# Performance work log

Hardware: AMD Instinct MI355X
Metric: run time of the kernel (lower is better)

## Reference

```python
import jax, jax.numpy as jnp
import numpy as np

FP8_MAX = 448.0  # max finite value of float8_e4m3fn
F8 = jnp.float8_e4m3fn


def setup_inputs() -> dict:
    key = jax.random.key(0)
    kx, kw, kb = jax.random.split(key, 3)
    B, S, K, N = 4, 2048, 4096, 16384
    x = jax.random.normal(kx, (B, S, K), dtype=jnp.float32)
    # Pre-quantized symmetric per-tensor FP8 weight: simulate quantization of a
    # realistically initialized fp32 weight with scale ws.
    ws = jnp.float32(0.01)
    w_fp32 = jax.random.normal(kw, (N, K), dtype=jnp.float32) * 0.02
    weight = jnp.clip(w_fp32 / ws, -FP8_MAX, FP8_MAX).astype(F8)  # [N, K] fp8
    weight_scale = jnp.full((1,), ws, dtype=jnp.float32)  # per-tensor strategy
    bias = jax.random.normal(kb, (N,), dtype=jnp.float32) * 0.01
    return {"x": x, "weight": weight, "weight_scale": weight_scale, "bias": bias}


def reference(x, weight, weight_scale, bias):
    # Dynamic per-tensor fp8 quantization of the activation (torchao
    # _input_activation_quant_func_fp8 with PerTensor granularity):
    # (input_scale * weight_scale), plus bias.
    amax = jnp.max(jnp.abs(x))
    x_scale = jnp.maximum(amax, jnp.float32(1e-12)) / FP8_MAX
    xq = jnp.clip(x / x_scale, -FP8_MAX, FP8_MAX).astype(F8).astype(jnp.float32)
    w = weight.astype(jnp.float32)  # [N, K]
    out = jnp.einsum("bsk,nk->bsn", xq, w)  # [B, S, N]
    out = out * (x_scale * weight_scale[0]) + bias
    return out
```

## Files before the change

kernel.cpp:

```cpp
#include <hip/hip_runtime.h>
#include <hip/hip_fp8.h>
#include <hip/hip_fp16.h>
#include <stdint.h>

#define FP8_MAX_V 448.0f

typedef float f32x16 __attribute__((ext_vector_type(16)));
typedef int i32x4 __attribute__((ext_vector_type(4)));
typedef int i32x8 __attribute__((ext_vector_type(8)));

__device__ __forceinline__ uint8_t cvt_fp8(float v) {
    return __hip_cvt_float_to_fp8(fminf(fmaxf(v, -FP8_MAX_V), FP8_MAX_V),
                                  __HIP_SATFINITE, __HIP_E4M3);
}

__global__ void fp8lin_init(unsigned* amax_bits) {
    *amax_bits = 0u;
}

__global__ void fp8lin_amax(const float4* __restrict__ x, unsigned* __restrict__ amax_bits, long n4) {
    float m = 0.f;
    long stride = (long)gridDim.x * blockDim.x;
    for (long i = blockIdx.x * (long)blockDim.x + threadIdx.x; i < n4; i += stride) {
        float4 v = x[i];
        m = fmaxf(m, fmaxf(fmaxf(fabsf(v.x), fabsf(v.y)), fmaxf(fabsf(v.z), fabsf(v.w))));
    }
#pragma unroll
    for (int o = 32; o; o >>= 1) m = fmaxf(m, __shfl_xor(m, o));
    if ((threadIdx.x & 63) == 0) atomicMax(amax_bits, __float_as_uint(m));
}

__global__ void fp8lin_scales(const unsigned* __restrict__ amax_bits,
                              const float* __restrict__ wscale,
                              float* __restrict__ scales) {
    float xs = fmaxf(__uint_as_float(*amax_bits), 1e-12f) / FP8_MAX_V;
    scales[0] = xs;
    scales[1] = xs * wscale[0];
}

__global__ void fp8lin_probe(const uint32_t* __restrict__ w, unsigned* __restrict__ flag) {
    __shared__ unsigned s32, s16, s4;
    if (threadIdx.x == 0) { s32 = 0u; s16 = 0u; s4 = 0u; }
    __syncthreads();
    unsigned o32 = 0u, o16 = 0u, o4 = 0u;
    for (int i = threadIdx.x; i < 4096; i += 256) {
        uint32_t v = w[i];
        o32 |= v & 0x000FFFFFu;
        uint32_t h0 = v & 0xFFFFu, h1 = v >> 16;
        o16 |= (h0 & 0x7Fu) | (h1 & 0x7Fu);
        o4  |= (h0 & 0x0Fu) | (h1 & 0x0Fu);
    }
    atomicOr(&s32, o32); atomicOr(&s16, o16); atomicOr(&s4, o4);
    __syncthreads();
    if (threadIdx.x == 0)
        *flag = (s32 == 0u) ? 0u : (s16 == 0u) ? 1u : (s4 == 0u) ? 2u : 3u;
}

__global__ void fp8lin_convw(const void* __restrict__ wsrc, const unsigned* __restrict__ flag,
                             uchar4* __restrict__ wq, long n4) {
    unsigned f = *flag;
    if (f == 3u) return;
    long stride = (long)gridDim.x * blockDim.x;
    if (f == 0u) {
        const float4* src = (const float4*)wsrc;
        for (long i = blockIdx.x * (long)blockDim.x + threadIdx.x; i < n4; i += stride) {
            float4 v = src[i];
            uchar4 o;
            o.x = cvt_fp8(v.x); o.y = cvt_fp8(v.y); o.z = cvt_fp8(v.z); o.w = cvt_fp8(v.w);
            wq[i] = o;
        }
    } else if (f == 1u) {
        const __half2* src = (const __half2*)wsrc;
        for (long i = blockIdx.x * (long)blockDim.x + threadIdx.x; i < n4; i += stride) {
            __half2 v0 = src[2 * i], v1 = src[2 * i + 1];
            uchar4 o;
            o.x = cvt_fp8(__half2float(v0.x)); o.y = cvt_fp8(__half2float(v0.y));
            o.z = cvt_fp8(__half2float(v1.x)); o.w = cvt_fp8(__half2float(v1.y));
            wq[i] = o;
        }
    } else {
        const ushort2* src = (const ushort2*)wsrc;
        for (long i = blockIdx.x * (long)blockDim.x + threadIdx.x; i < n4; i += stride) {
            ushort2 v0 = src[2 * i], v1 = src[2 * i + 1];
            uchar4 o;
            o.x = cvt_fp8(__uint_as_float((uint32_t)v0.x << 16));
            o.y = cvt_fp8(__uint_as_float((uint32_t)v0.y << 16));
            o.z = cvt_fp8(__uint_as_float((uint32_t)v1.x << 16));
            o.w = cvt_fp8(__uint_as_float((uint32_t)v1.y << 16));
            wq[i] = o;
        }
    }
}

__global__ void fp8lin_quant(const float4* __restrict__ x, const float* __restrict__ scales,
                             uchar4* __restrict__ xq, long n4) {
    float s = scales[0];
    long stride = (long)gridDim.x * blockDim.x;
    for (long i = blockIdx.x * (long)blockDim.x + threadIdx.x; i < n4; i += stride) {
        float4 v = x[i];
        uchar4 o;
        o.x = cvt_fp8(v.x / s); o.y = cvt_fp8(v.y / s);
        o.z = cvt_fp8(v.z / s); o.w = cvt_fp8(v.w / s);
        xq[i] = o;
    }
}

#define BM 256
#define BN 128
#define BK 64
#define A_BYTES 16384
#define B_BYTES 8192
#define BUF_BYTES (A_BYTES + B_BYTES)
#define SMEM_BYTES (2 * BUF_BYTES)

__device__ __forceinline__ void gload16(const uint8_t* src, uint8_t* ldst) {
    __builtin_amdgcn_global_load_lds(
        (const __attribute__((address_space(1))) uint32_t*)(uintptr_t)src,
        (__attribute__((address_space(3))) uint32_t*)(uintptr_t)ldst, 16, 0, 0);
}

#define WAITVM(N) asm volatile("s_waitcnt vmcnt(" #N ")" ::: "memory")
#define BARRIER() do { asm volatile("" ::: "memory"); __builtin_amdgcn_s_barrier(); \
                       asm volatile("" ::: "memory"); } while (0)

#define LDFRAG(dst, base, off) do {                                    \
    i32x4 _lo = *(const i32x4*)((base) + (off));                       \
    i32x4 _hi = *(const i32x4*)((base) + ((off) ^ 16));                \
    dst[0] = _lo[0]; dst[1] = _lo[1]; dst[2] = _lo[2]; dst[3] = _lo[3];\
    dst[4] = _hi[0]; dst[5] = _hi[1]; dst[6] = _hi[2]; dst[7] = _hi[3];\
} while (0)

#define MFMA_MX(A, B, C) __builtin_amdgcn_mfma_scale_f32_32x32x64_f8f6f4( \
    (A), (B), (C), 0, 0, 0, (int)0x7f7f7f7f, 0, (int)0x7f7f7f7f)

__global__ __launch_bounds__(256, 2) void fp8lin_gemm(
    const uint8_t* __restrict__ Aq,
    const uint8_t* __restrict__ Wraw,
    const uint8_t* __restrict__ Wconv,
    const unsigned* __restrict__ flag,
    const float* __restrict__ scales,
    const float* __restrict__ bias,
    float* __restrict__ out,
    int M, int N, int K) {
    extern __shared__ __align__(16) uint8_t smem[];

    const uint8_t* __restrict__ Wq = (*flag == 3u) ? Wraw : Wconv;

    const int tid = threadIdx.x;
    const int wid = tid >> 6;
    const int lane = tid & 63;
    const int wm = wid >> 1;
    const int wn = wid & 1;

    const int nbx = gridDim.x;
    const int orig = blockIdx.y * nbx + blockIdx.x;
    const int cpx = (gridDim.x * gridDim.y) >> 3;
    const int swzb = (orig & 7) * cpx + (orig >> 3);
    const int brow = (swzb / nbx) * BM;
    const int bcol = (swzb % nbx) * BN;

    const uint8_t* srcA[4];
    const uint8_t* srcB[2];
#pragma unroll
    for (int j = 0; j < 4; ++j) {
        int c = tid + 256 * j;
        int r = c >> 2;
        int sc = ((c & 3) ^ ((r >> 1) & 3)) * 16;
        srcA[j] = Aq + (size_t)(brow + r) * K + sc;
    }
#pragma unroll
    for (int j = 0; j < 2; ++j) {
        int c = tid + 256 * j;
        int r = c >> 2;
        int sc = ((c & 3) ^ ((r >> 1) & 3)) * 16;
        srcB[j] = Wq + (size_t)(bcol + r) * K + sc;
    }
    const int ldsW = wid * 1024;

    const int l31 = lane & 31;
    const int q = lane >> 5;
    const int swzr = (l31 >> 1) & 3;
    const int posl = (2 * q) ^ swzr;
    const int offA = (wm * 128 + l31) * 64 + posl * 16;
    const int offB = (wn * 64 + l31) * 64 + posl * 16;

    f32x16 acc[4][2];
#pragma unroll
    for (int mi = 0; mi < 4; ++mi)
#pragma unroll
        for (int ni = 0; ni < 2; ++ni)
#pragma unroll
            for (int r = 0; r < 16; ++r) acc[mi][ni][r] = 0.0f;

    auto STAGE = [&](int t, int ib) {
        size_t k0 = (size_t)t * BK;
        uint8_t* base = smem + ib * BUF_BYTES;
        gload16(srcA[0] + k0, base + ldsW);
        gload16(srcA[1] + k0, base + ldsW + 4096);
        gload16(srcA[2] + k0, base + ldsW + 8192);
        gload16(srcA[3] + k0, base + ldsW + 12288);
        gload16(srcB[0] + k0, base + A_BYTES + ldsW);
        gload16(srcB[1] + k0, base + A_BYTES + ldsW + 4096);
    };

    auto COMPUTE = [&](int ib) {
        const uint8_t* bA = smem + ib * BUF_BYTES;
        const uint8_t* bB = bA + A_BYTES;
        i32x8 a0, a1, a2, a3, b0, b1;
        LDFRAG(a0, bA, offA);
        LDFRAG(a1, bA, offA + 2048);
        LDFRAG(b0, bB, offB);
        LDFRAG(b1, bB, offB + 2048);
        __builtin_amdgcn_s_setprio(1);
        acc[0][0] = MFMA_MX(a0, b0, acc[0][0]);
        acc[1][0] = MFMA_MX(a1, b0, acc[1][0]);
        acc[0][1] = MFMA_MX(a0, b1, acc[0][1]);
        acc[1][1] = MFMA_MX(a1, b1, acc[1][1]);
        __builtin_amdgcn_s_setprio(0);
        LDFRAG(a2, bA, offA + 4096);
        LDFRAG(a3, bA, offA + 6144);
        __builtin_amdgcn_s_setprio(1);
        acc[2][0] = MFMA_MX(a2, b0, acc[2][0]);
        acc[3][0] = MFMA_MX(a3, b0, acc[3][0]);
        acc[2][1] = MFMA_MX(a2, b1, acc[2][1]);
        acc[3][1] = MFMA_MX(a3, b1, acc[3][1]);
        __builtin_amdgcn_s_setprio(0);
    };

    const int NT = K / BK;
    STAGE(0, 0);
    int cur = 0;
    for (int t = 0; t < NT - 1; ++t) {
        STAGE(t + 1, cur ^ 1);
        WAITVM(6);
        BARRIER();
        COMPUTE(cur);
        BARRIER();
        cur ^= 1;
    }
    WAITVM(0);
    BARRIER();
    COMPUTE(cur);

    float s = scales[1];
    const int colg = bcol + wn * 64 + l31;
    const int rowg0 = brow + wm * 128 + 4 * q;
#pragma unroll
    for (int ni = 0; ni < 2; ++ni) {
        int col = colg + ni * 32;
        float bv = bias[col];
#pragma unroll
        for (int mi = 0; mi < 4; ++mi) {
            int rb = rowg0 + mi * 32;
#pragma unroll
            for (int reg = 0; reg < 16; ++reg) {
                int row = rb + (reg & 3) + 8 * (reg >> 2);
                __builtin_nontemporal_store(acc[mi][ni][reg] * s + bv,
                                            out + (size_t)row * N + col);
            }
        }
    }
}

extern "C" void kernel_launch(void* const* d_in, const int* in_sizes, int n_in,
                              void* d_out, int out_size, void* d_ws, size_t ws_size,
                              hipStream_t stream) {
    const float* x = (const float*)d_in[0];
    const void* w = d_in[1];
    const float* wscale = (const float*)d_in[2];
    const float* bias = (const float*)d_in[3];
    float* out = (float*)d_out;

    const int Bb = 4, S = 2048, K = 4096, N = 16384;
    const int M = Bb * S;
    const long nx = (long)M * K;
    const long nw = (long)N * K;

    unsigned* amax_bits = (unsigned*)d_ws;
    float* scales = (float*)((char*)d_ws + 16);
    unsigned* wflag = (unsigned*)((char*)d_ws + 32);
    uchar4* xq = (uchar4*)((char*)d_ws + 256);
    uchar4* wq = (uchar4*)((char*)d_ws + 256 + nx);

    fp8lin_init<<<1, 1, 0, stream>>>(amax_bits);
    fp8lin_probe<<<1, 256, 0, stream>>>((const uint32_t*)w, wflag);
    fp8lin_amax<<<2048, 256, 0, stream>>>((const float4*)x, amax_bits, nx / 4);
    fp8lin_scales<<<1, 1, 0, stream>>>(amax_bits, wscale, scales);
    fp8lin_quant<<<2048, 256, 0, stream>>>((const float4*)x, scales, xq, nx / 4);
    fp8lin_convw<<<2048, 256, 0, stream>>>(w, wflag, wq, nw / 4);

    dim3 grid(N / BN, M / BM);
    fp8lin_gemm<<<grid, 256, SMEM_BYTES, stream>>>((const uint8_t*)xq, (const uint8_t*)w,
                                                   (const uint8_t*)wq, wflag, scales, bias, out,
                                                   M, N, K);
}
```

Before: 778.5 us.

## Load weight fragments directly from global into registers, bypassing LDS

The B (weight) tile no longer goes through shared memory. Each lane now loads its own MFMA fragment straight from global memory into registers, double-buffered across even and odd k-steps, while A stays staged in LDS. This halves LDS usage per block and removes the B LDS reads, but each B element is now fetched redundantly by the two wm warps. It also relies on uncoalesced per-lane 32-byte global reads and raises register pressure.

```diff
diff --git a/kernel.cpp b/kernel.cpp
--- a/kernel.cpp
+++ b/kernel.cpp
@@ -108,9 +108,8 @@
 #define BM 256
 #define BN 128
 #define BK 64
-#define A_BYTES 16384
-#define B_BYTES 8192
-#define BUF_BYTES (A_BYTES + B_BYTES)
+#define A_TILE 16384
+#define BUF_BYTES A_TILE
 #define SMEM_BYTES (2 * BUF_BYTES)
 
 __device__ __forceinline__ void gload16(const uint8_t* src, uint8_t* ldst) {
@@ -128,6 +127,14 @@
     i32x4 _hi = *(const i32x4*)((base) + ((off) ^ 16));                \
     dst[0] = _lo[0]; dst[1] = _lo[1]; dst[2] = _lo[2]; dst[3] = _lo[3];\
     dst[4] = _hi[0]; dst[5] = _hi[1]; dst[6] = _hi[2]; dst[7] = _hi[3];\
+} while (0)
+
+#define LOADB(bv, src, koff) do {                                      \
+    const uint8_t* _p = (src) + (koff);                                \
+    i32x4 _l0 = *(const i32x4*)(_p);                                   \
+    i32x4 _l1 = *(const i32x4*)(_p + 16);                              \
+    bv[0] = _l0[0]; bv[1] = _l0[1]; bv[2] = _l0[2]; bv[3] = _l0[3];    \
+    bv[4] = _l1[0]; bv[5] = _l1[1]; bv[6] = _l1[2]; bv[7] = _l1[3];    \
 } while (0)
 
 #define MFMA_MX(A, B, C) __builtin_amdgcn_mfma_scale_f32_32x32x64_f8f6f4( \
@@ -160,7 +167,6 @@
     const int bcol = (swzb % nbx) * BN;
 
     const uint8_t* srcA[4];
-    const uint8_t* srcB[2];
 #pragma unroll
     for (int j = 0; j < 4; ++j) {
         int c = tid + 256 * j;
@@ -168,13 +174,6 @@
         int sc = ((c & 3) ^ ((r >> 1) & 3)) * 16;
         srcA[j] = Aq + (size_t)(brow + r) * K + sc;
     }
-#pragma unroll
-    for (int j = 0; j < 2; ++j) {
-        int c = tid + 256 * j;
-        int r = c >> 2;
-        int sc = ((c & 3) ^ ((r >> 1) & 3)) * 16;
-        srcB[j] = Wq + (size_t)(bcol + r) * K + sc;
-    }
     const int ldsW = wid * 1024;
 
     const int l31 = lane & 31;
@@ -182,7 +181,9 @@
     const int swzr = (l31 >> 1) & 3;
     const int posl = (2 * q) ^ swzr;
     const int offA = (wm * 128 + l31) * 64 + posl * 16;
-    const int offB = (wn * 64 + l31) * 64 + posl * 16;
+
+    const uint8_t* srcB0 = Wq + (size_t)(bcol + wn * 64 + l31) * K + 32 * q;
+    const uint8_t* srcB1 = srcB0 + (size_t)32 * K;
 
     f32x16 acc[4][2];
 #pragma unroll
@@ -192,25 +193,20 @@
 #pragma unroll
             for (int r = 0; r < 16; ++r) acc[mi][ni][r] = 0.0f;
 
-    auto STAGE = [&](int t, int ib) {
+    auto STAGEA = [&](int t, int ib) {
         size_t k0 = (size_t)t * BK;
         uint8_t* base = smem + ib * BUF_BYTES;
         gload16(srcA[0] + k0, base + ldsW);
         gload16(srcA[1] + k0, base + ldsW + 4096);
         gload16(srcA[2] + k0, base + ldsW + 8192);
         gload16(srcA[3] + k0, base + ldsW + 12288);
-        gload16(srcB[0] + k0, base + A_BYTES + ldsW);
-        gload16(srcB[1] + k0, base + A_BYTES + ldsW + 4096);
     };
 
-    auto COMPUTE = [&](int ib) {
+    auto COMPUTE = [&](int ib, const i32x8& b0, const i32x8& b1) {
         const uint8_t* bA = smem + ib * BUF_BYTES;
-        const uint8_t* bB = bA + A_BYTES;
-        i32x8 a0, a1, a2, a3, b0, b1;
+        i32x8 a0, a1, a2, a3;
         LDFRAG(a0, bA, offA);
         LDFRAG(a1, bA, offA + 2048);
-        LDFRAG(b0, bB, offB);
-        LDFRAG(b1, bB, offB + 2048);
         __builtin_amdgcn_s_setprio(1);
         acc[0][0] = MFMA_MX(a0, b0, acc[0][0]);
         acc[1][0] = MFMA_MX(a1, b0, acc[1][0]);
@@ -228,19 +224,29 @@
     };
 
     const int NT = K / BK;
-    STAGE(0, 0);
-    int cur = 0;
-    for (int t = 0; t < NT - 1; ++t) {
-        STAGE(t + 1, cur ^ 1);
-        WAITVM(6);
+    i32x8 bE0, bE1, bO0, bO1;
+    LOADB(bE0, srcB0, 0); LOADB(bE1, srcB1, 0);
+    STAGEA(0, 0);
+    for (int tp = 0; tp < NT; tp += 2) {
+        LOADB(bO0, srcB0, (size_t)(tp + 1) * BK);
+        LOADB(bO1, srcB1, (size_t)(tp + 1) * BK);
+        STAGEA(tp + 1, 1);
+        WAITVM(8);
         BARRIER();
-        COMPUTE(cur);
+        COMPUTE(0, bE0, bE1);
         BARRIER();
-        cur ^= 1;
-    }
-    WAITVM(0);
-    BARRIER();
-    COMPUTE(cur);
+        if (tp + 2 < NT) {
+            LOADB(bE0, srcB0, (size_t)(tp + 2) * BK);
+            LOADB(bE1, srcB1, (size_t)(tp + 2) * BK);
+            STAGEA(tp + 2, 0);
+            WAITVM(8);
+        } else {
+            WAITVM(0);
+        }
+        BARRIER();
+        COMPUTE(1, bO0, bO1);
+        BARRIER();
+    }
 
     float s = scales[1];
     const int colg = bcol + wn * 64 + l31;
```

New measurement: 935.2 us. 1.2x slower.
